# Performance work log

Hardware: AMD Instinct MI355X
Metric: run time of the kernel (lower is better)

Reference implementation:

```python
import jax, jax.numpy as jnp
import numpy as np

ALPHA = 0.1        # self.alpha in the torch module
NUM_CLASSES = 10   # predict_acc hardcodes range(10)


def _sqdist(x, centers):
    # Faithful to sum((x - c)**2, -1) but computed via the gemm identity to
    # avoid materializing the (N, K, D) broadcast the torch code creates.
    x2 = jnp.sum(x * x, axis=1, keepdims=True)          # [N, 1]
    c2 = jnp.sum(centers * centers, axis=1)             # [K]
    d = x2 + c2[None, :] - 2.0 * (x @ centers.T)        # [N, K]
    return jnp.maximum(d, 0.0)                          # clamp fp round-off


def _predict_acc(distance, y):
    n = distance.shape[0]
    y_p = jnp.argmin(distance, axis=1)                  # index[1][:, 0]
    # counts[i, c] = #points assigned to cluster i (only i < 10 matter) with label c
    onehot_cluster = (y_p[:, None] == jnp.arange(NUM_CLASSES)[None, :]).astype(jnp.float32)  # [N, 10]
    onehot_label = (y[:, None] == jnp.arange(NUM_CLASSES)[None, :]).astype(jnp.float32)      # [N, 10]
    counts = onehot_cluster.T @ onehot_label            # [10, 10]
    used = jnp.zeros((NUM_CLASSES,), dtype=bool)
    correct = jnp.float32(0.0)
    for i in range(NUM_CLASSES):
        bin_i = counts[i]
        has_points = jnp.sum(bin_i) > 0                 # empty bincount -> 'continue'
        label = jnp.argmax(bin_i)                       # first max index, like where(bin==max)[0][0]
        # quchong: recursively zero already-used labels == argmax with used masked out
        masked = jnp.where(used, 0.0, bin_i)
        label = jnp.where(used[label], jnp.argmax(masked), label)
        correct = correct + jnp.where(has_points, bin_i[label], 0.0)
        used = jnp.where(has_points, used.at[label].set(True), used)
    return correct / jnp.float32(n)


def setup_inputs() -> dict:
    key = jax.random.key(0)
    kx, ky, kc = jax.random.split(key, 3)
    N, K, D = 262144, 256, 64
    x = jax.random.normal(kx, (N, D), dtype=jnp.float32)
    y = jax.random.randint(ky, (N,), 0, 10, dtype=jnp.int64)
    centers = jax.random.normal(kc, (K, D), dtype=jnp.float32)
    return {"x": x, "y": y, "centers": centers}


def reference(x, y, centers):
    distance = _sqdist(x, centers)                      # caldis, op='l2'
    # calwei: exp(-alpha*log(d+1)) then row-normalize
    we = jnp.exp(-ALPHA * jnp.log1p(distance))
    weight = we / jnp.sum(we, axis=1, keepdims=True)
    loss = jnp.sum(weight * distance)                   # calloss
    acc = _predict_acc(distance, y)
    return (loss, acc)
```

## Files before the change

### kernel.cpp

```cpp
#include <hip/hip_runtime.h>

#define ALPHA 0.1f
#define NUM_CLASSES 10

typedef __attribute__((ext_vector_type(8))) short bf16x8;
typedef __attribute__((ext_vector_type(4))) float f32x4;


__device__ __forceinline__ unsigned pack2(float a, float b) {
    return (__float_as_uint(b) & 0xFFFF0000u) | (__float_as_uint(a) >> 16);
}
__device__ __forceinline__ float truncbf(float a) {
    return __uint_as_float(__float_as_uint(a) & 0xFFFF0000u);
}

__global__ __launch_bounds__(512, 4) void dist_kernel(
    const float* __restrict__ x,
    const int*   __restrict__ y,
    const float* __restrict__ centers,
    float* __restrict__ loss_acc,
    unsigned int* __restrict__ counts,
    int NT)
{
    __shared__ __align__(16) char bstage[8 * 4 * 64 * 16];
    __shared__ float x2s[128];
    __shared__ float c2s[256];
    __shared__ float    comb_swe[8][128];
    __shared__ float    comb_swd[8][128];
    __shared__ unsigned comb_best[8][128];
    __shared__ unsigned counts_l[100];

    const int tid  = threadIdx.x;
    const int w    = tid >> 6;
    const int lane = tid & 63;
    const int q    = lane >> 4;
    const int r    = lane & 15;

    if (tid < 100) counts_l[tid] = 0u;

    if (tid < 256) {
        const float4* crow = (const float4*)(centers + tid * 64);
        float s = 0.f;
#pragma unroll
        for (int j = 0; j < 16; ++j) {
            float4 v = crow[j];
            s = fmaf(v.x, v.x, s); s = fmaf(v.y, v.y, s);
            s = fmaf(v.z, v.z, s); s = fmaf(v.w, v.w, s);
        }
        c2s[tid] = s;
    }

    bf16x8 af[2][4];
#pragma unroll
    for (int ct = 0; ct < 2; ++ct) {
        const int row = w * 32 + ct * 16 + r;
        const float4* C = (const float4*)(centers + (size_t)row * 64);
        float4 v0 = C[q * 2], v1 = C[q * 2 + 1];
        float4 v2 = C[8 + q * 2], v3 = C[9 + q * 2];
        float4 m0 = make_float4(-2.f * v0.x, -2.f * v0.y, -2.f * v0.z, -2.f * v0.w);
        float4 m1 = make_float4(-2.f * v1.x, -2.f * v1.y, -2.f * v1.z, -2.f * v1.w);
        float4 m2 = make_float4(-2.f * v2.x, -2.f * v2.y, -2.f * v2.z, -2.f * v2.w);
        float4 m3 = make_float4(-2.f * v3.x, -2.f * v3.y, -2.f * v3.z, -2.f * v3.w);
        union { bf16x8 v; unsigned u[4]; } h0, h1, l0, l1;
        h0.u[0] = pack2(m0.x, m0.y); h0.u[1] = pack2(m0.z, m0.w);
        h0.u[2] = pack2(m1.x, m1.y); h0.u[3] = pack2(m1.z, m1.w);
        h1.u[0] = pack2(m2.x, m2.y); h1.u[1] = pack2(m2.z, m2.w);
        h1.u[2] = pack2(m3.x, m3.y); h1.u[3] = pack2(m3.z, m3.w);
        l0.u[0] = pack2(m0.x - truncbf(m0.x), m0.y - truncbf(m0.y));
        l0.u[1] = pack2(m0.z - truncbf(m0.z), m0.w - truncbf(m0.w));
        l0.u[2] = pack2(m1.x - truncbf(m1.x), m1.y - truncbf(m1.y));
        l0.u[3] = pack2(m1.z - truncbf(m1.z), m1.w - truncbf(m1.w));
        l1.u[0] = pack2(m2.x - truncbf(m2.x), m2.y - truncbf(m2.y));
        l1.u[1] = pack2(m2.z - truncbf(m2.z), m2.w - truncbf(m2.w));
        l1.u[2] = pack2(m3.x - truncbf(m3.x), m3.y - truncbf(m3.y));
        l1.u[3] = pack2(m3.z - truncbf(m3.z), m3.w - truncbf(m3.w));
        af[ct][0] = h0.v; af[ct][1] = h1.v; af[ct][2] = l0.v; af[ct][3] = l1.v;
    }

    float4 pv0, pv1, pv2, pv3;
    {
        const int row = blockIdx.x * 128 + w * 16 + r;
        const float4* X = (const float4*)(x + (size_t)row * 64);
        pv0 = X[q * 2]; pv1 = X[q * 2 + 1];
        pv2 = X[8 + q * 2]; pv3 = X[9 + q * 2];
    }

    __syncthreads();

    float c2r1[2][4];
#pragma unroll
    for (int ct = 0; ct < 2; ++ct) {
        float4 v = *(const float4*)(c2s + w * 32 + ct * 16 + q * 4);
        c2r1[ct][0] = v.x + 1.f; c2r1[ct][1] = v.y + 1.f;
        c2r1[ct][2] = v.z + 1.f; c2r1[ct][3] = v.w + 1.f;
    }

    float loss_local = 0.f;

    for (int t = blockIdx.x; t < NT; t += gridDim.x) {
        int ylab = 0;
        if (tid < 128) ylab = y[t * 128 + tid];

        {
            float4 v0 = pv0, v1 = pv1, v2 = pv2, v3 = pv3;

            const int tn = t + gridDim.x;
            if (tn < NT) {
                const int row = tn * 128 + w * 16 + r;
                const float4* X = (const float4*)(x + (size_t)row * 64);
                pv0 = X[q * 2]; pv1 = X[q * 2 + 1];
                pv2 = X[8 + q * 2]; pv3 = X[9 + q * 2];
            }

            float p = v0.x * v0.x;
            p = fmaf(v0.y, v0.y, p); p = fmaf(v0.z, v0.z, p); p = fmaf(v0.w, v0.w, p);
            p = fmaf(v1.x, v1.x, p); p = fmaf(v1.y, v1.y, p); p = fmaf(v1.z, v1.z, p); p = fmaf(v1.w, v1.w, p);
            p = fmaf(v2.x, v2.x, p); p = fmaf(v2.y, v2.y, p); p = fmaf(v2.z, v2.z, p); p = fmaf(v2.w, v2.w, p);
            p = fmaf(v3.x, v3.x, p); p = fmaf(v3.y, v3.y, p); p = fmaf(v3.z, v3.z, p); p = fmaf(v3.w, v3.w, p);
            p += __shfl_xor(p, 16);
            p += __shfl_xor(p, 32);
            if (q == 0) x2s[w * 16 + r] = p;

            union { bf16x8 v; uint4 u4; unsigned u[4]; } h0, h1, l0, l1;
            h0.u[0] = pack2(v0.x, v0.y); h0.u[1] = pack2(v0.z, v0.w);
            h0.u[2] = pack2(v1.x, v1.y); h0.u[3] = pack2(v1.z, v1.w);
            h1.u[0] = pack2(v2.x, v2.y); h1.u[1] = pack2(v2.z, v2.w);
            h1.u[2] = pack2(v3.x, v3.y); h1.u[3] = pack2(v3.z, v3.w);
            l0.u[0] = pack2(v0.x - truncbf(v0.x), v0.y - truncbf(v0.y));
            l0.u[1] = pack2(v0.z - truncbf(v0.z), v0.w - truncbf(v0.w));
            l0.u[2] = pack2(v1.x - truncbf(v1.x), v1.y - truncbf(v1.y));
            l0.u[3] = pack2(v1.z - truncbf(v1.z), v1.w - truncbf(v1.w));
            l1.u[0] = pack2(v2.x - truncbf(v2.x), v2.y - truncbf(v2.y));
            l1.u[1] = pack2(v2.z - truncbf(v2.z), v2.w - truncbf(v2.w));
            l1.u[2] = pack2(v3.x - truncbf(v3.x), v3.y - truncbf(v3.y));
            l1.u[3] = pack2(v3.z - truncbf(v3.z), v3.w - truncbf(v3.w));
            *(uint4*)(bstage + (((w * 4 + 0) * 64 + lane) << 4)) = h0.u4;
            *(uint4*)(bstage + (((w * 4 + 1) * 64 + lane) << 4)) = h1.u4;
            *(uint4*)(bstage + (((w * 4 + 2) * 64 + lane) << 4)) = l0.u4;
            *(uint4*)(bstage + (((w * 4 + 3) * 64 + lane) << 4)) = l1.u4;
        }
        __syncthreads();

#pragma unroll
        for (int pt = 0; pt < 8; ++pt) {
            union { uint4 u4; bf16x8 v; } b0, b1, b2, b3;
            b0.u4 = *(const uint4*)(bstage + (((pt * 4 + 0) * 64 + lane) << 4));
            b1.u4 = *(const uint4*)(bstage + (((pt * 4 + 1) * 64 + lane) << 4));
            b2.u4 = *(const uint4*)(bstage + (((pt * 4 + 2) * 64 + lane) << 4));
            b3.u4 = *(const uint4*)(bstage + (((pt * 4 + 3) * 64 + lane) << 4));
            const float x2p = x2s[pt * 16 + r];

            f32x4 acc[2];
#pragma unroll
            for (int ct = 0; ct < 2; ++ct) {
                f32x4 a;
                a[0] = x2p + c2r1[ct][0]; a[1] = x2p + c2r1[ct][1];
                a[2] = x2p + c2r1[ct][2]; a[3] = x2p + c2r1[ct][3];
                a = __builtin_amdgcn_mfma_f32_16x16x32_bf16(af[ct][0], b0.v, a, 0, 0, 0);
                a = __builtin_amdgcn_mfma_f32_16x16x32_bf16(af[ct][1], b1.v, a, 0, 0, 0);
                a = __builtin_amdgcn_mfma_f32_16x16x32_bf16(af[ct][2], b0.v, a, 0, 0, 0);
                a = __builtin_amdgcn_mfma_f32_16x16x32_bf16(af[ct][3], b1.v, a, 0, 0, 0);
                a = __builtin_amdgcn_mfma_f32_16x16x32_bf16(af[ct][0], b2.v, a, 0, 0, 0);
                a = __builtin_amdgcn_mfma_f32_16x16x32_bf16(af[ct][1], b3.v, a, 0, 0, 0);
                acc[ct] = a;
            }

            float swe = 0.f, swdu = 0.f;
            unsigned best = 0xFFFFFFFFu;
#pragma unroll
            for (int ct = 0; ct < 2; ++ct) {
#pragma unroll
                for (int reg = 0; reg < 4; ++reg) {
                    const float u = acc[ct][reg];
                    const unsigned kid = (unsigned)(w * 32 + ct * 16 + q * 4 + reg);
                    best = min(best, (__float_as_uint(u) & 0xFFFFFF00u) | kid);
                    float wg = exp2f(-ALPHA * __log2f(u));
                    swe += wg;
                    swdu = fmaf(wg, u, swdu);
                }
            }
            swe += __shfl_xor(swe, 16); swe += __shfl_xor(swe, 32);
            swdu += __shfl_xor(swdu, 16); swdu += __shfl_xor(swdu, 32);
            best = min(best, (unsigned)__shfl_xor((int)best, 16));
            best = min(best, (unsigned)__shfl_xor((int)best, 32));
            if (q == 0) {
                comb_swe[w][pt * 16 + r]  = swe;
                comb_swd[w][pt * 16 + r]  = swdu;
                comb_best[w][pt * 16 + r] = best;
            }
        }
        __syncthreads();

        if (tid < 128) {
            float SWE = comb_swe[0][tid], SWD = comb_swd[0][tid];
            unsigned BEST = comb_best[0][tid];
#pragma unroll
            for (int g = 1; g < 8; ++g) {
                SWE += comb_swe[g][tid];
                SWD += comb_swd[g][tid];
                BEST = min(BEST, comb_best[g][tid]);
            }
            loss_local += SWD / SWE - 1.f;
            const unsigned bk = BEST & 0xFFu;
            if (bk < NUM_CLASSES) {
                atomicAdd(&counts_l[bk * NUM_CLASSES + ylab], 1u);
            }
        }
    }

    if (w < 2) {
        float v = loss_local;
#pragma unroll
        for (int o = 32; o > 0; o >>= 1) v += __shfl_down(v, o);
        if (lane == 0) atomicAdd(loss_acc, v);
    }

    __syncthreads();
    if (tid < 100) {
        const unsigned c = counts_l[tid];
        if (c) atomicAdd(&counts[tid], c);
    }
}


__global__ void finalize_kernel(
    const float* __restrict__ loss_acc,
    const unsigned int* __restrict__ counts,
    float* __restrict__ out,
    int N)
{
    if (threadIdx.x == 0 && blockIdx.x == 0) {
        float c[NUM_CLASSES][NUM_CLASSES];
        for (int i = 0; i < NUM_CLASSES; ++i)
            for (int j = 0; j < NUM_CLASSES; ++j)
                c[i][j] = (float)counts[i * NUM_CLASSES + j];

        bool used[NUM_CLASSES];
        for (int i = 0; i < NUM_CLASSES; ++i) used[i] = false;

        float correct = 0.f;
        for (int i = 0; i < NUM_CLASSES; ++i) {
            float rowsum = 0.f;
            for (int j = 0; j < NUM_CLASSES; ++j) rowsum += c[i][j];
            bool has_points = rowsum > 0.f;

            int label = 0;
            float mx = c[i][0];
            for (int j = 1; j < NUM_CLASSES; ++j)
                if (c[i][j] > mx) { mx = c[i][j]; label = j; }

            if (used[label]) {
                float mm = used[0] ? 0.f : c[i][0];
                int l2 = 0;
                for (int j = 1; j < NUM_CLASSES; ++j) {
                    float v = used[j] ? 0.f : c[i][j];
                    if (v > mm) { mm = v; l2 = j; }
                }
                label = l2;
            }

            if (has_points) {
                correct += c[i][label];
                used[label] = true;
            }
        }
        out[0] = loss_acc[0];
        out[1] = correct / (float)N;
    }
}


extern "C" void kernel_launch(void* const* d_in, const int* in_sizes, int n_in,
                              void* d_out, int out_size, void* d_ws, size_t ws_size,
                              hipStream_t stream)
{
    const float* x       = (const float*)d_in[0];
    const int*   y       = (const int*)d_in[1];
    const float* centers = (const float*)d_in[2];
    float* out = (float*)d_out;

    const int N  = in_sizes[0] / 64;
    const int NT = N / 128;

    float* loss          = (float*)d_ws;
    unsigned int* counts = (unsigned int*)((char*)d_ws + 4);

    hipMemsetAsync(d_ws, 0, 512, stream);

    int grid = 1024;
    if (grid > NT) grid = NT;
    dist_kernel<<<grid, 512, 0, stream>>>(x, y, centers, loss, counts, NT);

    finalize_kernel<<<1, 64, 0, stream>>>(loss, counts, out, N);
}
```

Baseline: 157.0 us.

## Split MFMA accumulator chains, flatten shuffle reductions, raise occupancy, parallelize finalize loads

Splits each chain of six dependent MFMAs into two independent accumulators that are summed at the end, shortening the dependency chain. Replaces the two-step xor-shuffle reductions with three direct shuffles per lane and restructures the per-row exp/log and argmin work into flatter trees. Raises the launch-bounds occupancy target from 4 to 6 and shrinks the grid from 1024 to 768 blocks. Finalize now loads the counts in parallel into shared memory before a single thread runs the assignment logic. The higher occupancy target may force register spills, and the changed summation order can shift float results slightly.

```diff
diff --git a/kernel.cpp b/kernel.cpp
--- a/kernel.cpp
+++ b/kernel.cpp
@@ -13,8 +13,20 @@
 __device__ __forceinline__ float truncbf(float a) {
     return __uint_as_float(__float_as_uint(a) & 0xFFFF0000u);
 }
-
-__global__ __launch_bounds__(512, 4) void dist_kernel(
+__device__ __forceinline__ float gsum4(float v, int s1, int s2, int s3) {
+    const float a = __shfl(v, s1);
+    const float b = __shfl(v, s2);
+    const float c = __shfl(v, s3);
+    return (v + a) + (b + c);
+}
+__device__ __forceinline__ unsigned gmin4(unsigned v, int s1, int s2, int s3) {
+    const unsigned a = (unsigned)__shfl((int)v, s1);
+    const unsigned b = (unsigned)__shfl((int)v, s2);
+    const unsigned c = (unsigned)__shfl((int)v, s3);
+    return min(min(v, a), min(b, c));
+}
+
+__global__ __launch_bounds__(512, 6) void dist_kernel(
     const float* __restrict__ x,
     const int*   __restrict__ y,
     const float* __restrict__ centers,
@@ -35,6 +47,7 @@
     const int lane = tid & 63;
     const int q    = lane >> 4;
     const int r    = lane & 15;
+    const int s1 = r + 16, s2 = r + 32, s3 = r + 48;
 
     if (tid < 100) counts_l[tid] = 0u;
 
@@ -117,8 +130,7 @@
             p = fmaf(v1.x, v1.x, p); p = fmaf(v1.y, v1.y, p); p = fmaf(v1.z, v1.z, p); p = fmaf(v1.w, v1.w, p);
             p = fmaf(v2.x, v2.x, p); p = fmaf(v2.y, v2.y, p); p = fmaf(v2.z, v2.z, p); p = fmaf(v2.w, v2.w, p);
             p = fmaf(v3.x, v3.x, p); p = fmaf(v3.y, v3.y, p); p = fmaf(v3.z, v3.z, p); p = fmaf(v3.w, v3.w, p);
-            p += __shfl_xor(p, 16);
-            p += __shfl_xor(p, 32);
+            p = gsum4(p, s1, s2, s3);
             if (q == 0) x2s[w * 16 + r] = p;
 
             union { bf16x8 v; uint4 u4; unsigned u[4]; } h0, h1, l0, l1;
@@ -153,36 +165,47 @@
             f32x4 acc[2];
 #pragma unroll
             for (int ct = 0; ct < 2; ++ct) {
-                f32x4 a;
-                a[0] = x2p + c2r1[ct][0]; a[1] = x2p + c2r1[ct][1];
-                a[2] = x2p + c2r1[ct][2]; a[3] = x2p + c2r1[ct][3];
-                a = __builtin_amdgcn_mfma_f32_16x16x32_bf16(af[ct][0], b0.v, a, 0, 0, 0);
-                a = __builtin_amdgcn_mfma_f32_16x16x32_bf16(af[ct][1], b1.v, a, 0, 0, 0);
-                a = __builtin_amdgcn_mfma_f32_16x16x32_bf16(af[ct][2], b0.v, a, 0, 0, 0);
-                a = __builtin_amdgcn_mfma_f32_16x16x32_bf16(af[ct][3], b1.v, a, 0, 0, 0);
-                a = __builtin_amdgcn_mfma_f32_16x16x32_bf16(af[ct][0], b2.v, a, 0, 0, 0);
-                a = __builtin_amdgcn_mfma_f32_16x16x32_bf16(af[ct][1], b3.v, a, 0, 0, 0);
-                acc[ct] = a;
-            }
-
-            float swe = 0.f, swdu = 0.f;
-            unsigned best = 0xFFFFFFFFu;
+                f32x4 aA;
+                aA[0] = x2p + c2r1[ct][0]; aA[1] = x2p + c2r1[ct][1];
+                aA[2] = x2p + c2r1[ct][2]; aA[3] = x2p + c2r1[ct][3];
+                f32x4 aB = {0.f, 0.f, 0.f, 0.f};
+                aA = __builtin_amdgcn_mfma_f32_16x16x32_bf16(af[ct][0], b0.v, aA, 0, 0, 0);
+                aB = __builtin_amdgcn_mfma_f32_16x16x32_bf16(af[ct][1], b1.v, aB, 0, 0, 0);
+                aA = __builtin_amdgcn_mfma_f32_16x16x32_bf16(af[ct][2], b0.v, aA, 0, 0, 0);
+                aB = __builtin_amdgcn_mfma_f32_16x16x32_bf16(af[ct][3], b1.v, aB, 0, 0, 0);
+                aA = __builtin_amdgcn_mfma_f32_16x16x32_bf16(af[ct][0], b2.v, aA, 0, 0, 0);
+                aB = __builtin_amdgcn_mfma_f32_16x16x32_bf16(af[ct][1], b3.v, aB, 0, 0, 0);
+                acc[ct] = aA + aB;
+            }
+
+            float swe_c[2], swd_c[2];
+            unsigned bst_c[2];
 #pragma unroll
             for (int ct = 0; ct < 2; ++ct) {
-#pragma unroll
-                for (int reg = 0; reg < 4; ++reg) {
-                    const float u = acc[ct][reg];
-                    const unsigned kid = (unsigned)(w * 32 + ct * 16 + q * 4 + reg);
-                    best = min(best, (__float_as_uint(u) & 0xFFFFFF00u) | kid);
-                    float wg = exp2f(-ALPHA * __log2f(u));
-                    swe += wg;
-                    swdu = fmaf(wg, u, swdu);
-                }
-            }
-            swe += __shfl_xor(swe, 16); swe += __shfl_xor(swe, 32);
-            swdu += __shfl_xor(swdu, 16); swdu += __shfl_xor(swdu, 32);
-            best = min(best, (unsigned)__shfl_xor((int)best, 16));
-            best = min(best, (unsigned)__shfl_xor((int)best, 32));
+                const float u0 = acc[ct][0], u1 = acc[ct][1];
+                const float u2 = acc[ct][2], u3 = acc[ct][3];
+                const unsigned kb = (unsigned)(w * 32 + ct * 16 + q * 4);
+                const unsigned p0 = (__float_as_uint(u0) & 0xFFFFFF00u) | kb;
+                const unsigned p1 = (__float_as_uint(u1) & 0xFFFFFF00u) | (kb + 1);
+                const unsigned p2 = (__float_as_uint(u2) & 0xFFFFFF00u) | (kb + 2);
+                const unsigned p3 = (__float_as_uint(u3) & 0xFFFFFF00u) | (kb + 3);
+                bst_c[ct] = min(min(p0, p1), min(p2, p3));
+                const float g0 = exp2f(-ALPHA * __log2f(u0));
+                const float g1 = exp2f(-ALPHA * __log2f(u1));
+                const float g2 = exp2f(-ALPHA * __log2f(u2));
+                const float g3 = exp2f(-ALPHA * __log2f(u3));
+                swe_c[ct] = (g0 + g1) + (g2 + g3);
+                float t0 = g0 * u0; t0 = fmaf(g1, u1, t0);
+                float t1 = g2 * u2; t1 = fmaf(g3, u3, t1);
+                swd_c[ct] = t0 + t1;
+            }
+            float swe = swe_c[0] + swe_c[1];
+            float swdu = swd_c[0] + swd_c[1];
+            unsigned best = min(bst_c[0], bst_c[1]);
+
+            swe  = gsum4(swe, s1, s2, s3);
+            swdu = gsum4(swdu, s1, s2, s3);
+            best = gmin4(best, s1, s2, s3);
             if (q == 0) {
                 comb_swe[w][pt * 16 + r]  = swe;
                 comb_swd[w][pt * 16 + r]  = swdu;
@@ -229,42 +252,44 @@
     float* __restrict__ out,
     int N)
 {
-    if (threadIdx.x == 0 && blockIdx.x == 0) {
-        float c[NUM_CLASSES][NUM_CLASSES];
-        for (int i = 0; i < NUM_CLASSES; ++i)
-            for (int j = 0; j < NUM_CLASSES; ++j)
-                c[i][j] = (float)counts[i * NUM_CLASSES + j];
-
+    __shared__ float cs[NUM_CLASSES * NUM_CLASSES];
+    __shared__ float ls;
+    const int tid = threadIdx.x;
+    if (tid < NUM_CLASSES * NUM_CLASSES) cs[tid] = (float)counts[tid];
+    if (tid == NUM_CLASSES * NUM_CLASSES) ls = loss_acc[0];
+    __syncthreads();
+    if (tid == 0) {
         bool used[NUM_CLASSES];
         for (int i = 0; i < NUM_CLASSES; ++i) used[i] = false;
 
         float correct = 0.f;
         for (int i = 0; i < NUM_CLASSES; ++i) {
+            const float* ci = cs + i * NUM_CLASSES;
             float rowsum = 0.f;
-            for (int j = 0; j < NUM_CLASSES; ++j) rowsum += c[i][j];
+            for (int j = 0; j < NUM_CLASSES; ++j) rowsum += ci[j];
             bool has_points = rowsum > 0.f;
 
             int label = 0;
-            float mx = c[i][0];
+            float mx = ci[0];
             for (int j = 1; j < NUM_CLASSES; ++j)
-                if (c[i][j] > mx) { mx = c[i][j]; label = j; }
+                if (ci[j] > mx) { mx = ci[j]; label = j; }
 
             if (used[label]) {
-                float mm = used[0] ? 0.f : c[i][0];
+                float mm = used[0] ? 0.f : ci[0];
                 int l2 = 0;
                 for (int j = 1; j < NUM_CLASSES; ++j) {
-                    float v = used[j] ? 0.f : c[i][j];
+                    float v = used[j] ? 0.f : ci[j];
                     if (v > mm) { mm = v; l2 = j; }
                 }
                 label = l2;
             }
 
             if (has_points) {
-                correct += c[i][label];
+                correct += ci[label];
                 used[label] = true;
             }
         }
-        out[0] = loss_acc[0];
+        out[0] = ls;
         out[1] = correct / (float)N;
     }
 }
@@ -287,9 +312,9 @@
 
     hipMemsetAsync(d_ws, 0, 512, stream);
 
-    int grid = 1024;
+    int grid = 768;
     if (grid > NT) grid = NT;
     dist_kernel<<<grid, 512, 0, stream>>>(x, y, centers, loss, counts, NT);
 
-    finalize_kernel<<<1, 64, 0, stream>>>(loss, counts, out, N);
-}
+    finalize_kernel<<<1, 128, 0, stream>>>(loss, counts, out, N);
+}
```

Measured after the change: 228.0 us. +45.3%, slower.
